# Optimization experiments

Hardware: AMD Instinct MI355X
Metric: run time of the kernel (lower is better)

Reference implementation:

```python
import jax, jax.numpy as jnp
import numpy as np

N_TOKENS, OUT, E, H, D = 32, 1, 768, 12, 8
B, L = 64, 256
DH = E // H


def layer_norm(x, g, b, eps=1e-5):
    mu = jnp.mean(x, axis=-1, keepdims=True)
    var = jnp.mean((x - mu) ** 2, axis=-1, keepdims=True)
    return (x - mu) * jax.lax.rsqrt(var + eps) * g + b


def setup_inputs() -> dict:
    key = jax.random.key(0)
    ks = jax.random.split(key, 16)
    tokens = jax.random.randint(ks[0], (B, L), 0, N_TOKENS)
    padding = jnp.zeros((B, L), dtype=bool)
    r = jax.random.normal(ks[1], (B, L, 3), dtype=jnp.float32) * 3.0
    s = 0.02
    embed = jax.random.normal(ks[2], (N_TOKENS, E), jnp.float32) * s
    embed = embed.at[0].set(0.0)  # padding_idx=0
    inp = dict(
        tokens=tokens, padding=padding, r=r, embed=embed,
        mu=jax.random.uniform(ks[3], (D, H), jnp.float32, 0.0, 4.0),
        gamma=jax.random.uniform(ks[4], (D, H), jnp.float32, 0.1, 1.0),
        w=jax.random.normal(ks[5], (D, H), jnp.float32),
        Wqkv=jax.random.normal(ks[6], (D, E, 3 * E), jnp.float32) * s,
        bqkv=jnp.zeros((D, 3 * E), jnp.float32),
        Wo=jax.random.normal(ks[7], (D, E, E), jnp.float32) * s,
        bo=jnp.zeros((D, E), jnp.float32),
        ln1_g=jnp.ones((D, E), jnp.float32), ln1_b=jnp.zeros((D, E), jnp.float32),
        W1=jax.random.normal(ks[8], (D, E, 4 * E), jnp.float32) * s,
        b1=jnp.zeros((D, 4 * E), jnp.float32),
        W2=jax.random.normal(ks[9], (D, 4 * E, E), jnp.float32) * s,
        b2=jnp.zeros((D, E), jnp.float32),
        ln2_g=jnp.ones((D, E), jnp.float32), ln2_b=jnp.zeros((D, E), jnp.float32),
        lnf_g=jnp.ones((E,), jnp.float32), lnf_b=jnp.zeros((E,), jnp.float32),
        Wout=jax.random.normal(ks[10], (E, OUT), jnp.float32) * s,
        bout=jnp.zeros((OUT,), jnp.float32),
    )
    return inp


def reference(tokens, padding, r, embed, mu, gamma, w, Wqkv, bqkv, Wo, bo,
              ln1_g, ln1_b, W1, b1, W2, b2, ln2_g, ln2_b, lnf_g, lnf_b, Wout, bout):
    Bc, Lc = tokens.shape
    # pairwise distances (eps for grad stability at d=0 on diagonal)
    diff = r[:, :, None, :] - r[:, None, :, :]              # [B,L,L,3]
    d = jnp.sqrt(jnp.sum(diff * diff, axis=-1) + 1e-12)     # [B,L,L]
    diag = jnp.eye(Lc, dtype=bool)
    pad_pair = padding[:, None, :] | padding[:, :, None]    # [B,L,L]
    attn_mask = (pad_pair | diag)[:, None, :, :]            # [B,1,L,L] True=blocked
    pad_e = padding[:, :, None]                              # [B,L,1]
    neg = jnp.asarray(-1e9, jnp.float32)

    e = embed[tokens]                                        # [B,L,E]
    scale = 1.0 / np.sqrt(DH)
    for i in range(D):
        # learned per-head Gaussian RBF attention bias
        bias = w[i][None, :, None, None] * jnp.exp(
            -gamma[i][None, :, None, None] * (d[:, None, :, :] - mu[i][None, :, None, None]) ** 2
        )                                                    # [B,H,L,L]
        e0 = layer_norm(e, ln1_g[i], ln1_b[i])
        qkv = e0 @ Wqkv[i] + bqkv[i]
        q, k, v = jnp.split(qkv, 3, axis=-1)
        q = q.reshape(Bc, Lc, H, DH).transpose(0, 2, 1, 3)
        k = k.reshape(Bc, Lc, H, DH).transpose(0, 2, 1, 3)
        v = v.reshape(Bc, Lc, H, DH).transpose(0, 2, 1, 3)
        scores = jnp.einsum('bhid,bhjd->bhij', q, k) * scale + bias
        scores = jnp.where(attn_mask, neg, scores)
        a = jax.nn.softmax(scores, axis=-1)
        o = jnp.einsum('bhij,bhjd->bhid', a, v)
        o = o.transpose(0, 2, 1, 3).reshape(Bc, Lc, E)
        e1 = o @ Wo[i] + bo[i]
        e2 = layer_norm(e1 + e0, ln2_g[i], ln2_b[i])
        e3 = jax.nn.relu(e2 @ W1[i] + b1[i]) @ W2[i] + b2[i]
        e3 = jnp.where(pad_e, 0.0, e3)
        e = e3 + e2
    e = layer_norm(e, lnf_g, lnf_b)
    e = jnp.mean(e, axis=1)
    return e @ Wout + bout
```

## Files before the change

kernel.cpp:

```cpp
#include <hip/hip_runtime.h>
#include <cstdint>
#include <cstddef>

#define B_    64
#define L_    256
#define E_    768
#define H_    12
#define DH_   64
#define D_    8
#define FF_   3072
#define QKV3_ 2304
#define M_    (B_*L_)

typedef _Float16 f16;
typedef f16   f16x8  __attribute__((ext_vector_type(8)));
typedef float f32x4  __attribute__((ext_vector_type(4)));

__device__ __forceinline__ void gl_lds16(const void* g, void* l){
    __builtin_amdgcn_global_load_lds(
        (const __attribute__((address_space(1))) void*)g,
        (__attribute__((address_space(3))) void*)l, 16, 0, 0);
}

__global__ void sentinel_kernel(float* out, int n){
    int i = blockIdx.x*64 + threadIdx.x;
    if (i < n) out[i] = 1.0e6f;
}

__global__ __launch_bounds__(256) void gather_kernel(
    const int* __restrict__ tok, const float* __restrict__ emb, float* __restrict__ e)
{
    const int idx = blockIdx.x*256 + threadIdx.x;
    const int row = idx / E_;
    const int d   = idx - row*E_;
    e[idx] = emb[(size_t)tok[row]*E_ + d];
}

__global__ void wsplit_kernel(const float* __restrict__ W, f16* __restrict__ Hh, int K, int N)
{
    __shared__ float tile[32][33];
    const int tx = threadIdx.x, ty = threadIdx.y;
#pragma unroll
    for (int i2 = 0; i2 < 4; ++i2){
        const int k = blockIdx.y*32 + ty + i2*8;
        const int n = blockIdx.x*32 + tx;
        tile[ty + i2*8][tx] = W[(size_t)k*N + n];
    }
    __syncthreads();
    const int k2 = blockIdx.y*32 + tx;
#pragma unroll
    for (int i2 = 0; i2 < 4; ++i2){
        const int n2 = blockIdx.x*32 + ty + i2*8;
        Hh[(size_t)n2*K + k2] = (f16)tile[tx][ty + i2*8];
    }
}

__global__ __launch_bounds__(256) void ln_kernel(
    const float* __restrict__ x, const float* __restrict__ g, const float* __restrict__ bb,
    float* __restrict__ yF, f16* __restrict__ yH, f16* __restrict__ yL)
{
    __shared__ float red[256];
    const int row = blockIdx.x, tid = threadIdx.x;
    const float* xr = x + (size_t)row*E_;
    float v0 = xr[tid], v1 = xr[tid+256], v2 = xr[tid+512];
    red[tid] = v0 + v1 + v2;
    __syncthreads();
    for (int o = 128; o; o >>= 1){ if (tid < o) red[tid] += red[tid+o]; __syncthreads(); }
    const float mean = red[0] * (1.f/768.f);
    __syncthreads();
    const float d0 = v0-mean, d1 = v1-mean, d2 = v2-mean;
    red[tid] = d0*d0 + d1*d1 + d2*d2;
    __syncthreads();
    for (int o = 128; o; o >>= 1){ if (tid < o) red[tid] += red[tid+o]; __syncthreads(); }
    const float rstd = rsqrtf(red[0]*(1.f/768.f) + 1e-5f);
    const float dv[3] = {d0, d1, d2};
#pragma unroll
    for (int q = 0; q < 3; ++q){
        const int d = tid + q*256;
        const float y = dv[q]*rstd*g[d] + bb[d];
        const size_t idx = (size_t)row*E_ + d;
        if (yF) yF[idx] = y;
        if (yH){
            const f16 hi = (f16)y;
            yH[idx] = hi;
            yL[idx] = (f16)(y - (float)hi);
        }
    }
}

template<int MODE>
__global__ __launch_bounds__(256, 3) void gemm_kernel(
    const f16* __restrict__ A, const f16* __restrict__ Bh,
    const float* __restrict__ bias,
    const f16* __restrict__ exH, const f16* __restrict__ exL,
    const unsigned char* __restrict__ pad,
    float* __restrict__ Cf, f16* __restrict__ Cq,
    f16* __restrict__ qh, f16* __restrict__ kh, f16* __restrict__ vt,
    int Mn, int Nn, int Kn)
{
    __shared__ f16 sA[3][128*32];
    __shared__ f16 sB[3][128*32];
    const int tid = threadIdx.x;
    const int w = tid >> 6, l = tid & 63;
    const int nt = gridDim.x;
    const int ypg = gridDim.y >> 3;
    const int f = blockIdx.y * nt + blockIdx.x;
    const int g = f >> 3;
    const int by = (f & 7) + 8 * (g % ypg);
    const int bx = g / ypg;
    const int m0 = by * 128, n0 = bx * 128;
    const int waveM = (w & 1) * 64, waveN = (w >> 1) * 64;
    const int fr = l & 15, fq = l >> 4;
    const int kswz = ((fq ^ ((fr >> 1) & 3)) << 3);
    f32x4 acc[4][4] = {};

    const int r0 = tid >> 2, j0 = tid & 3;
    const int r1 = r0 + 64;
    const int j0s = j0 ^ ((r0 >> 1) & 3);
    const int j1s = j0 ^ ((r1 >> 1) & 3);
    const f16* pa0 = A  + (size_t)(m0 + r0) * Kn + j0s*8;
    const f16* pa1 = A  + (size_t)(m0 + r1) * Kn + j1s*8;
    const f16* pb0 = Bh + (size_t)(n0 + r0) * Kn + j0s*8;
    const f16* pb1 = Bh + (size_t)(n0 + r1) * Kn + j1s*8;
    const int d0 = tid*8, d1 = tid*8 + 2048;

#define STAGE_(U, KK) do { \
        const size_t ko_ = (size_t)(KK) * 32; \
        gl_lds16(pa0 + ko_, &sA[U][d0]); \
        gl_lds16(pa1 + ko_, &sA[U][d1]); \
        gl_lds16(pb0 + ko_, &sB[U][d0]); \
        gl_lds16(pb1 + ko_, &sB[U][d1]); \
    } while(0)

#define COMPUTE_(U) do { \
        f16x8 fa[4], fb[4]; \
        _Pragma("unroll") \
        for (int m = 0; m < 4; ++m){ \
            fa[m] = *(const f16x8*)&sA[U][(waveM + m*16 + fr)*32 + kswz]; \
            fb[m] = *(const f16x8*)&sB[U][(waveN + m*16 + fr)*32 + kswz]; \
        } \
        __builtin_amdgcn_s_setprio(1); \
        _Pragma("unroll") \
        for (int m = 0; m < 4; ++m) \
        _Pragma("unroll") \
        for (int n = 0; n < 4; ++n) \
            acc[m][n] = __builtin_amdgcn_mfma_f32_16x16x32_f16(fa[m], fb[n], acc[m][n], 0,0,0); \
        __builtin_amdgcn_s_setprio(0); \
    } while(0)

#define WAITV4 asm volatile("s_waitcnt vmcnt(4)" ::: "memory")
#define WAITV0 asm volatile("s_waitcnt vmcnt(0)" ::: "memory")
#define BAR_   do { asm volatile("" ::: "memory"); __builtin_amdgcn_s_barrier(); asm volatile("" ::: "memory"); } while(0)

    const int ns = Kn >> 5;
    STAGE_(0, 0);
    STAGE_(1, 1);
    for (int s = 0; s < ns; s += 3){
#pragma unroll
        for (int u = 0; u < 3; ++u){
            const int st = s + u;
            if (st + 1 < ns) WAITV4; else WAITV0;
            BAR_;
            if (st + 2 < ns) STAGE_((u + 2) % 3, st + 2);
            COMPUTE_(u);
        }
    }
#undef STAGE_
#undef COMPUTE_
#undef WAITV4
#undef WAITV0
#undef BAR_

#pragma unroll
    for (int jt = 0; jt < 4; ++jt){
        const int col = n0 + waveN + jt*16 + fr;
        const float bc = bias[col];
        int which = 0, hh = 0, dd = 0;
        if (MODE == 0){
            which = col / 768;
            const int hc = col - which*768;
            hh = hc >> 6; dd = hc & 63;
        }
#pragma unroll
        for (int it = 0; it < 4; ++it)
#pragma unroll
            for (int rg = 0; rg < 4; ++rg){
                const int row = m0 + waveM + it*16 + fq*4 + rg;
                float v = acc[it][jt][rg] + bc;
                if (MODE == 0){
                    const int bb2 = row >> 8, jj2 = row & 255;
                    const size_t bh = (size_t)bb2 * H_ + hh;
                    if (which == 0)      qh[(bh*256 + jj2)*64 + dd] = (f16)v;
                    else if (which == 1) kh[(bh*256 + jj2)*64 + dd] = (f16)v;
                    else                 vt[(bh*64 + dd)*256 + jj2] = (f16)v;
                } else {
                    const size_t idx = (size_t)row * Nn + col;
                    if (MODE == 1){
                        Cf[idx] = v + (float)exH[idx] + (float)exL[idx];
                    } else if (MODE == 2){
                        Cq[idx] = (f16)fmaxf(v, 0.f);
                    } else {
                        if (pad[row]) v = 0.f;
                        Cf[idx] = v + (float)exH[idx] + (float)exL[idx];
                    }
                }
            }
    }
}

__global__ __launch_bounds__(256, 4) void attn_kernel(
    const f16* __restrict__ qh, const f16* __restrict__ kh, const f16* __restrict__ vt,
    const float* __restrict__ rpos, const unsigned char* __restrict__ pad,
    const float* __restrict__ mu, const float* __restrict__ ga, const float* __restrict__ wv,
    f16* __restrict__ o)
{
    __shared__ f16 sK[64*72];
    __shared__ f16 sV[64*72];
    __shared__ f16 sP[4][16*72];
    __shared__ float rx[256], ry[256], rz[256], pf[256];

    const int h = blockIdx.x, b = blockIdx.y, p = blockIdx.z;
    const int tid = threadIdx.x, w = tid >> 6, l = tid & 63;
    const int fr = l & 15, fq = l >> 4;
    const float muh = mu[h], gah = ga[h], wh = wv[h];
    const size_t bh = (size_t)b * H_ + h;
    const int rowbase = b * L_;

    rx[tid] = rpos[(size_t)(rowbase+tid)*3 + 0];
    ry[tid] = rpos[(size_t)(rowbase+tid)*3 + 1];
    rz[tid] = rpos[(size_t)(rowbase+tid)*3 + 2];
    pf[tid] = pad[rowbase+tid] ? 1.f : 0.f;

    f16x8 fQ[2];
    {
        const int r = p*64 + w*16 + fr;
        const f16* qp = qh + (bh*256 + r)*64 + fq*8;
        fQ[0] = *(const f16x8*)(qp);
        fQ[1] = *(const f16x8*)(qp + 32);
    }

    float m_[4], l_[4];
    f32x4 oacc[4] = {};
#pragma unroll
    for (int rg = 0; rg < 4; ++rg){ m_[rg] = -3.0e38f; l_[rg] = 0.f; }
    __syncthreads();

    for (int c = 0; c < 4; ++c){
        __syncthreads();
        {
            const int e0 = tid*8, e1 = e0 + 2048;
            const int kr0 = e0 >> 6, kd0 = e0 & 63;
            const int kr1 = e1 >> 6, kd1 = e1 & 63;
            *(uint4*)&sK[kr0*72 + kd0] = *(const uint4*)&kh[(bh*256 + c*64 + kr0)*64 + kd0];
            *(uint4*)&sK[kr1*72 + kd1] = *(const uint4*)&kh[(bh*256 + c*64 + kr1)*64 + kd1];
            *(uint4*)&sV[kr0*72 + kd0] = *(const uint4*)&vt[(bh*64 + kr0)*256 + c*64 + kd0];
            *(uint4*)&sV[kr1*72 + kd1] = *(const uint4*)&vt[(bh*64 + kr1)*256 + c*64 + kd1];
        }
        __syncthreads();
        f32x4 sacc[4] = {};
#pragma unroll
        for (int nt = 0; nt < 4; ++nt)
#pragma unroll
            for (int kf = 0; kf < 2; ++kf){
                const f16x8 fb = *(const f16x8*)&sK[(nt*16 + fr)*72 + kf*32 + fq*8];
                sacc[nt] = __builtin_amdgcn_mfma_f32_16x16x32_f16(fQ[kf], fb, sacc[nt], 0,0,0);
            }
        float sv[4][4];
        float rmax[4] = {-3.0e38f, -3.0e38f, -3.0e38f, -3.0e38f};
        const int ibase = p*64 + w*16 + fq*4;
#pragma unroll
        for (int nt = 0; nt < 4; ++nt){
            const int j = c*64 + nt*16 + fr;
            const float jx = rx[j], jy = ry[j], jz = rz[j], jp = pf[j];
#pragma unroll
            for (int rg = 0; rg < 4; ++rg){
                const int i = ibase + rg;
                const float dx = rx[i]-jx, dy = ry[i]-jy, dz = rz[i]-jz;
                const float dist = sqrtf(dx*dx + dy*dy + dz*dz + 1e-12f);
                const float t = dist - muh;
                float s = sacc[nt][rg]*0.125f + wh*__expf(-gah*t*t);
                if ((j == i) | (pf[i] != 0.f) | (jp != 0.f)) s = -1e9f;
                sv[nt][rg] = s;
                rmax[rg] = fmaxf(rmax[rg], s);
            }
        }
#pragma unroll
        for (int rg = 0; rg < 4; ++rg){
#pragma unroll
            for (int off = 8; off >= 1; off >>= 1)
                rmax[rg] = fmaxf(rmax[rg], __shfl_xor(rmax[rg], off));
            const float mnew = fmaxf(m_[rg], rmax[rg]);
            const float alpha = __expf(m_[rg] - mnew);
            m_[rg] = mnew;
            l_[rg] *= alpha;
#pragma unroll
            for (int dt = 0; dt < 4; ++dt) oacc[dt][rg] *= alpha;
            float rs = 0.f;
#pragma unroll
            for (int nt = 0; nt < 4; ++nt){
                const float pv = __expf(sv[nt][rg] - mnew);
                sP[w][(fq*4 + rg)*72 + nt*16 + fr] = (f16)pv;
                rs += pv;
            }
#pragma unroll
            for (int off = 8; off >= 1; off >>= 1) rs += __shfl_xor(rs, off);
            l_[rg] += rs;
        }
#pragma unroll
        for (int kf = 0; kf < 2; ++kf){
            const f16x8 pa = *(const f16x8*)&sP[w][fr*72 + kf*32 + fq*8];
#pragma unroll
            for (int dt = 0; dt < 4; ++dt){
                const f16x8 vb = *(const f16x8*)&sV[(dt*16 + fr)*72 + kf*32 + fq*8];
                oacc[dt] = __builtin_amdgcn_mfma_f32_16x16x32_f16(pa, vb, oacc[dt], 0,0,0);
            }
        }
    }
    const int rglob = rowbase + p*64 + w*16 + fq*4;
#pragma unroll
    for (int rg = 0; rg < 4; ++rg){
        const float inv = 1.f / l_[rg];
#pragma unroll
        for (int dt = 0; dt < 4; ++dt)
            o[(size_t)(rglob + rg)*E_ + h*64 + dt*16 + fr] = (f16)(oacc[dt][rg]*inv);
    }
}

__global__ __launch_bounds__(256) void mean_kernel(const float* __restrict__ x, float* __restrict__ m)
{
    const int b = blockIdx.x, tid = threadIdx.x;
    const float* xb = x + (size_t)b*L_*E_;
#pragma unroll
    for (int q = 0; q < 3; ++q){
        const int d = tid + q*256;
        float s = 0.f;
        for (int l2 = 0; l2 < L_; ++l2) s += xb[(size_t)l2*E_ + d];
        m[b*E_ + d] = s * (1.f/(float)L_);
    }
}

__global__ __launch_bounds__(256) void out_kernel(
    const float* __restrict__ m, const float* __restrict__ Wout,
    const float* __restrict__ bout, float* __restrict__ out)
{
    __shared__ float red[256];
    const int b = blockIdx.x, tid = threadIdx.x;
    float s = 0.f;
#pragma unroll
    for (int q = 0; q < 3; ++q){ const int d = tid + q*256; s += m[b*E_ + d]*Wout[d]; }
    red[tid] = s;
    __syncthreads();
    for (int o = 128; o; o >>= 1){ if (tid < o) red[tid] += red[tid+o]; __syncthreads(); }
    if (tid == 0) out[b] = red[0] + bout[0];
}

extern "C" void kernel_launch(void* const* d_in, const int* in_sizes, int n_in,
                              void* d_out, int out_size, void* d_ws, size_t ws_size,
                              hipStream_t stream)
{
    const int*            tokens  = (const int*)d_in[0];
    const unsigned char*  padding = (const unsigned char*)d_in[1];
    const float*          rpos    = (const float*)d_in[2];
    const float*          embed   = (const float*)d_in[3];
    const float*          mu      = (const float*)d_in[4];
    const float*          ga      = (const float*)d_in[5];
    const float*          wv      = (const float*)d_in[6];
    const float*          Wqkv    = (const float*)d_in[7];
    const float*          bqkv    = (const float*)d_in[8];
    const float*          Wo      = (const float*)d_in[9];
    const float*          bo      = (const float*)d_in[10];
    const float*          ln1g    = (const float*)d_in[11];
    const float*          ln1b    = (const float*)d_in[12];
    const float*          W1      = (const float*)d_in[13];
    const float*          b1      = (const float*)d_in[14];
    const float*          W2      = (const float*)d_in[15];
    const float*          b2      = (const float*)d_in[16];
    const float*          ln2g    = (const float*)d_in[17];
    const float*          ln2b    = (const float*)d_in[18];
    const float*          lnfg    = (const float*)d_in[19];
    const float*          lnfb    = (const float*)d_in[20];
    const float*          Wout    = (const float*)d_in[21];
    const float*          bout    = (const float*)d_in[22];
    float* out = (float*)d_out;
    (void)in_sizes; (void)n_in;

    char* ws = (char*)d_ws;
    size_t off = 0;
    auto alloc = [&](size_t bytes)->char*{
        char* p = ws + off;
        off += (bytes + 255) & ~(size_t)255;
        return p;
    };
    const size_t PLANE = (size_t)M_*E_;
    float* e     = (float*)alloc(PLANE*4);
    char*  big   = alloc(PLANE*2*4);
    f16*   actH  = (f16*)alloc(PLANE*2);
    f16*   actL  = (f16*)alloc(PLANE*2);
    f16*   wqh   = (f16*)alloc((size_t)E_*QKV3_*2);
    f16*   woh   = (f16*)alloc((size_t)E_*E_*2);
    f16*   w1h   = (f16*)alloc((size_t)E_*FF_*2);
    f16*   w2h   = (f16*)alloc((size_t)FF_*E_*2);
    float* meanb = (float*)alloc((size_t)B_*E_*4);
    const size_t required = off;

    if (ws_size < required){
        sentinel_kernel<<<dim3((out_size+63)/64), dim3(64), 0, stream>>>(out, out_size);
        return;
    }

    f16*   qh   = (f16*)big;
    f16*   kh   = qh + PLANE;
    f16*   vt   = kh + PLANE;
    f16*   ob   = vt + PLANE;
    f16*   hbuf = (f16*)big;
    float* lnfo = (float*)big;
    float* sbuf = e;

    gather_kernel<<<dim3(M_*E_/256), dim3(256), 0, stream>>>(tokens, embed, e);

    for (int i = 0; i < D_; ++i){
        wsplit_kernel<<<dim3(QKV3_/32, E_/32), dim3(32,8), 0, stream>>>(
            Wqkv + (size_t)i*E_*QKV3_, wqh, E_, QKV3_);
        wsplit_kernel<<<dim3(E_/32, E_/32), dim3(32,8), 0, stream>>>(
            Wo + (size_t)i*E_*E_, woh, E_, E_);
        wsplit_kernel<<<dim3(FF_/32, E_/32), dim3(32,8), 0, stream>>>(
            W1 + (size_t)i*E_*FF_, w1h, E_, FF_);
        wsplit_kernel<<<dim3(E_/32, FF_/32), dim3(32,8), 0, stream>>>(
            W2 + (size_t)i*FF_*E_, w2h, FF_, E_);

        ln_kernel<<<dim3(M_), dim3(256), 0, stream>>>(e, ln1g + i*E_, ln1b + i*E_, nullptr, actH, actL);
        gemm_kernel<0><<<dim3(QKV3_/128, M_/128), dim3(256), 0, stream>>>(
            actH, wqh, bqkv + i*QKV3_, nullptr, nullptr, nullptr,
            nullptr, nullptr, qh, kh, vt, M_, QKV3_, E_);
        attn_kernel<<<dim3(H_, B_, 4), dim3(256), 0, stream>>>(
            qh, kh, vt, rpos, padding, mu + i*H_, ga + i*H_, wv + i*H_, ob);
        gemm_kernel<1><<<dim3(E_/128, M_/128), dim3(256), 0, stream>>>(
            ob, woh, bo + i*E_, actH, actL, nullptr,
            sbuf, nullptr, nullptr, nullptr, nullptr, M_, E_, E_);
        ln_kernel<<<dim3(M_), dim3(256), 0, stream>>>(sbuf, ln2g + i*E_, ln2b + i*E_, nullptr, actH, actL);
        gemm_kernel<2><<<dim3(FF_/128, M_/128), dim3(256), 0, stream>>>(
            actH, w1h, b1 + i*FF_, nullptr, nullptr, nullptr,
            nullptr, hbuf, nullptr, nullptr, nullptr, M_, FF_, E_);
        gemm_kernel<3><<<dim3(E_/128, M_/128), dim3(256), 0, stream>>>(
            hbuf, w2h, b2 + i*E_, actH, actL, padding,
            e, nullptr, nullptr, nullptr, nullptr, M_, E_, FF_);
    }

    ln_kernel<<<dim3(M_), dim3(256), 0, stream>>>(e, lnfg, lnfb, lnfo, nullptr, nullptr);
    mean_kernel<<<dim3(B_), dim3(256), 0, stream>>>(lnfo, meanb);
    out_kernel<<<dim3(B_), dim3(256), 0, stream>>>(meanb, Wout, bout, out);
}
```

Baseline: 4.305 ms.

## Switch GEMM tiles to 128x192 with three waves each owning full M

Changes the GEMM block tile from 128x128 with four 2x2 waves to 128x192 with three waves, each computing 128 rows by 64 columns. The A and B tiles share one LDS ring buffer, and each wave issues seven direct-to-LDS loads per stage. Each wave now reads all eight A fragments per k-step, raising MFMA count per LDS read and reducing B-tile passes over A. The trade-offs are a larger accumulator register footprint, lower occupancy (launch bounds now 192 threads, 2 blocks), and fewer blocks per GEMM.

```diff
diff --git a/kernel.cpp b/kernel.cpp
--- a/kernel.cpp
+++ b/kernel.cpp
@@ -89,7 +89,7 @@
 }
 
 template<int MODE>
-__global__ __launch_bounds__(256, 3) void gemm_kernel(
+__global__ __launch_bounds__(192, 2) void gemm_kernel(
     const f16* __restrict__ A, const f16* __restrict__ Bh,
     const float* __restrict__ bias,
     const f16* __restrict__ exH, const f16* __restrict__ exL,
@@ -98,8 +98,7 @@
     f16* __restrict__ qh, f16* __restrict__ kh, f16* __restrict__ vt,
     int Mn, int Nn, int Kn)
 {
-    __shared__ f16 sA[3][128*32];
-    __shared__ f16 sB[3][128*32];
+    __shared__ f16 ring[3][10240];
     const int tid = threadIdx.x;
     const int w = tid >> 6, l = tid & 63;
     const int nt = gridDim.x;
@@ -108,47 +107,55 @@
     const int g = f >> 3;
     const int by = (f & 7) + 8 * (g % ypg);
     const int bx = g / ypg;
-    const int m0 = by * 128, n0 = bx * 128;
-    const int waveM = (w & 1) * 64, waveN = (w >> 1) * 64;
+    const int m0 = by * 128, n0 = bx * 192;
     const int fr = l & 15, fq = l >> 4;
     const int kswz = ((fq ^ ((fr >> 1) & 3)) << 3);
-    f32x4 acc[4][4] = {};
-
-    const int r0 = tid >> 2, j0 = tid & 3;
-    const int r1 = r0 + 64;
-    const int j0s = j0 ^ ((r0 >> 1) & 3);
-    const int j1s = j0 ^ ((r1 >> 1) & 3);
-    const f16* pa0 = A  + (size_t)(m0 + r0) * Kn + j0s*8;
-    const f16* pa1 = A  + (size_t)(m0 + r1) * Kn + j1s*8;
-    const f16* pb0 = Bh + (size_t)(n0 + r0) * Kn + j0s*8;
-    const f16* pb1 = Bh + (size_t)(n0 + r1) * Kn + j1s*8;
-    const int d0 = tid*8, d1 = tid*8 + 2048;
+    f32x4 acc[8][4] = {};
+
+    const int rl = l >> 2, jj = l & 3;
+    const f16* gp[7];
+    int ldo[7];
+#pragma unroll
+    for (int i = 0; i < 7; ++i){
+        int s = w*7 + i; if (s > 19) s = 19;
+        ldo[i] = s*512 + l*8;
+        if (s < 8){
+            const int row = s*16 + rl;
+            const int js  = jj ^ ((row >> 1) & 3);
+            gp[i] = A + (size_t)(m0 + row) * Kn + js*8;
+        } else {
+            const int row = (s - 8)*16 + rl;
+            const int js  = jj ^ ((row >> 1) & 3);
+            gp[i] = Bh + (size_t)(n0 + row) * Kn + js*8;
+        }
+    }
 
 #define STAGE_(U, KK) do { \
         const size_t ko_ = (size_t)(KK) * 32; \
-        gl_lds16(pa0 + ko_, &sA[U][d0]); \
-        gl_lds16(pa1 + ko_, &sA[U][d1]); \
-        gl_lds16(pb0 + ko_, &sB[U][d0]); \
-        gl_lds16(pb1 + ko_, &sB[U][d1]); \
+        _Pragma("unroll") \
+        for (int i = 0; i < 7; ++i) \
+            gl_lds16(gp[i] + ko_, &ring[U][ldo[i]]); \
     } while(0)
 
 #define COMPUTE_(U) do { \
-        f16x8 fa[4], fb[4]; \
+        f16x8 fb[4]; \
         _Pragma("unroll") \
-        for (int m = 0; m < 4; ++m){ \
-            fa[m] = *(const f16x8*)&sA[U][(waveM + m*16 + fr)*32 + kswz]; \
-            fb[m] = *(const f16x8*)&sB[U][(waveN + m*16 + fr)*32 + kswz]; \
-        } \
+        for (int n = 0; n < 4; ++n) \
+            fb[n] = *(const f16x8*)&ring[U][4096 + (w*64 + n*16 + fr)*32 + kswz]; \
+        f16x8 fa[8]; \
+        _Pragma("unroll") \
+        for (int m = 0; m < 8; ++m) \
+            fa[m] = *(const f16x8*)&ring[U][(m*16 + fr)*32 + kswz]; \
         __builtin_amdgcn_s_setprio(1); \
         _Pragma("unroll") \
-        for (int m = 0; m < 4; ++m) \
+        for (int m = 0; m < 8; ++m) \
         _Pragma("unroll") \
         for (int n = 0; n < 4; ++n) \
             acc[m][n] = __builtin_amdgcn_mfma_f32_16x16x32_f16(fa[m], fb[n], acc[m][n], 0,0,0); \
         __builtin_amdgcn_s_setprio(0); \
     } while(0)
 
-#define WAITV4 asm volatile("s_waitcnt vmcnt(4)" ::: "memory")
+#define WAITV7 asm volatile("s_waitcnt vmcnt(7)" ::: "memory")
 #define WAITV0 asm volatile("s_waitcnt vmcnt(0)" ::: "memory")
 #define BAR_   do { asm volatile("" ::: "memory"); __builtin_amdgcn_s_barrier(); asm volatile("" ::: "memory"); } while(0)
 
@@ -159,7 +166,7 @@
 #pragma unroll
         for (int u = 0; u < 3; ++u){
             const int st = s + u;
-            if (st + 1 < ns) WAITV4; else WAITV0;
+            if (st + 1 < ns) WAITV7; else WAITV0;
             BAR_;
             if (st + 2 < ns) STAGE_((u + 2) % 3, st + 2);
             COMPUTE_(u);
@@ -167,13 +174,13 @@
     }
 #undef STAGE_
 #undef COMPUTE_
-#undef WAITV4
+#undef WAITV7
 #undef WAITV0
 #undef BAR_
 
 #pragma unroll
     for (int jt = 0; jt < 4; ++jt){
-        const int col = n0 + waveN + jt*16 + fr;
+        const int col = n0 + w*64 + jt*16 + fr;
         const float bc = bias[col];
         int which = 0, hh = 0, dd = 0;
         if (MODE == 0){
@@ -182,10 +189,10 @@
             hh = hc >> 6; dd = hc & 63;
         }
 #pragma unroll
-        for (int it = 0; it < 4; ++it)
+        for (int it = 0; it < 8; ++it)
 #pragma unroll
             for (int rg = 0; rg < 4; ++rg){
-                const int row = m0 + waveM + it*16 + fq*4 + rg;
+                const int row = m0 + it*16 + fq*4 + rg;
                 float v = acc[it][jt][rg] + bc;
                 if (MODE == 0){
                     const int bb2 = row >> 8, jj2 = row & 255;
@@ -429,19 +436,19 @@
             W2 + (size_t)i*FF_*E_, w2h, FF_, E_);
 
         ln_kernel<<<dim3(M_), dim3(256), 0, stream>>>(e, ln1g + i*E_, ln1b + i*E_, nullptr, actH, actL);
-        gemm_kernel<0><<<dim3(QKV3_/128, M_/128), dim3(256), 0, stream>>>(
+        gemm_kernel<0><<<dim3(QKV3_/192, M_/128), dim3(192), 0, stream>>>(
             actH, wqh, bqkv + i*QKV3_, nullptr, nullptr, nullptr,
             nullptr, nullptr, qh, kh, vt, M_, QKV3_, E_);
         attn_kernel<<<dim3(H_, B_, 4), dim3(256), 0, stream>>>(
             qh, kh, vt, rpos, padding, mu + i*H_, ga + i*H_, wv + i*H_, ob);
-        gemm_kernel<1><<<dim3(E_/128, M_/128), dim3(256), 0, stream>>>(
+        gemm_kernel<1><<<dim3(E_/192, M_/128), dim3(192), 0, stream>>>(
             ob, woh, bo + i*E_, actH, actL, nullptr,
             sbuf, nullptr, nullptr, nullptr, nullptr, M_, E_, E_);
         ln_kernel<<<dim3(M_), dim3(256), 0, stream>>>(sbuf, ln2g + i*E_, ln2b + i*E_, nullptr, actH, actL);
-        gemm_kernel<2><<<dim3(FF_/128, M_/128), dim3(256), 0, stream>>>(
+        gemm_kernel<2><<<dim3(FF_/192, M_/128), dim3(192), 0, stream>>>(
             actH, w1h, b1 + i*FF_, nullptr, nullptr, nullptr,
             nullptr, hbuf, nullptr, nullptr, nullptr, M_, FF_, E_);
-        gemm_kernel<3><<<dim3(E_/128, M_/128), dim3(256), 0, stream>>>(
+        gemm_kernel<3><<<dim3(E_/192, M_/128), dim3(192), 0, stream>>>(
             hbuf, w2h, b2 + i*E_, actH, actL, padding,
             e, nullptr, nullptr, nullptr, nullptr, M_, E_, FF_);
     }
```

Result: slower. 4.998 ms (+16.1%).
